# Kernel tuning notes

Measured on AMD Instinct MI355X. Metric: run time of the kernel, lower is better.

The kernel has to match this reference:

```python
import jax, jax.numpy as jnp
import numpy as np

B = 8192          # batch rows
F0 = 2048         # base input features
E = 512           # embed rows added per recursion level
L = 3             # chain depth
OUT = 2048        # MAIN output dim
NNZ_E = 8192      # nnz per embed sparse weight (~16/row)
NNZ_M = 16384     # nnz of MAIN sparse weight (~8/row)


def _spmm_t(rows, cols, vals, x, n_rows):
    """Compute (W_sparse @ x.T).T = x @ W.T for COO W of shape [n_rows, x.shape[1]].
    out[b, r] = sum_{k: rows[k]==r} vals[k] * x[b, cols[k]]
    """
    contrib = x[:, cols] * vals                     # [B, nnz]
    return jax.ops.segment_sum(contrib.T, rows, num_segments=n_rows).T  # [B, n_rows]


def setup_inputs() -> dict:
    key = jax.random.key(0)
    ks = jax.random.split(key, 12)
    widths = [F0, F0 + E, F0 + 2 * E]               # input width at each recursion level
    inp = {"x": jax.random.normal(ks[0], (B, F0), dtype=jnp.float32)}
    for i, w in enumerate(widths):
        inp[f"emb_rows{i}"] = jax.random.randint(ks[1 + 3 * i], (NNZ_E,), 0, E, dtype=jnp.int32)
        inp[f"emb_cols{i}"] = jax.random.randint(ks[2 + 3 * i], (NNZ_E,), 0, w, dtype=jnp.int32)
        inp[f"emb_vals{i}"] = jax.random.normal(ks[3 + 3 * i], (NNZ_E,), dtype=jnp.float32)
    inp["main_rows"] = jax.random.randint(ks[10], (NNZ_M,), 0, OUT, dtype=jnp.int32)
    inp["main_cols"] = jax.random.randint(ks[11], (NNZ_M,), 0, F0 + 3 * E, dtype=jnp.int32)
    inp["main_vals"] = jax.random.normal(jax.random.fold_in(key, 99), (NNZ_M,), dtype=jnp.float32)
    return inp


def reference(x, emb_rows0, emb_cols0, emb_vals0,
              emb_rows1, emb_cols1, emb_vals1,
              emb_rows2, emb_cols2, emb_vals2,
              main_rows, main_cols, main_vals):
    # Recursive chain unrolled oldest-first: each level sparse-mms its embed
    # weight against the running input and concatenates the result.
    h = x
    for rows, cols, vals in ((emb_rows0, emb_cols0, emb_vals0),
                             (emb_rows1, emb_cols1, emb_vals1),
                             (emb_rows2, emb_cols2, emb_vals2)):
        e = _spmm_t(rows, cols, vals, h, E)         # [B, E]
        h = jnp.concatenate([h, e], axis=1)
    # is_last: pass concatenated features through the MAIN sparse linear
    return _spmm_t(main_rows, main_cols, main_vals, h, OUT)  # [B, OUT]
```

## Files before the change

### kernel.cpp

```cpp
#include <hip/hip_runtime.h>
#include <stdint.h>

#define F0    2048
#define EROWS 512
#define NOUT  2048
#define MROWS 8192

typedef __attribute__((ext_vector_type(8))) short bf16x8;
typedef __attribute__((ext_vector_type(4))) float f32x4;
typedef __attribute__((ext_vector_type(8))) unsigned short u16x8;

typedef const __attribute__((address_space(1))) unsigned char ga_t;
typedef __attribute__((address_space(3))) unsigned char lds_t;

__device__ __forceinline__ void async_load16(const void* g, void* l) {
  __builtin_amdgcn_global_load_lds((ga_t*)g, (lds_t*)l, 16, 0, 0);
}

__device__ __forceinline__ unsigned short f2bf(float f) {
  unsigned int u = __builtin_bit_cast(unsigned int, f);
  u += 0x7fffu + ((u >> 16) & 1u);
  return (unsigned short)(u >> 16);
}

__global__ __launch_bounds__(256) void csr_cast_kernel(
    const int* __restrict__ r0, const int* __restrict__ c0, const float* __restrict__ v0, int n0,
    const int* __restrict__ r1, const int* __restrict__ c1, const float* __restrict__ v1, int n1,
    const int* __restrict__ r2, const int* __restrict__ c2, const float* __restrict__ v2, int n2,
    const int* __restrict__ rm, const int* __restrict__ cm, const float* __restrict__ vm, int nm,
    int* __restrict__ rp_all, int* __restrict__ cc_all, float* __restrict__ cv_all,
    const float* __restrict__ x, unsigned short* __restrict__ Ab)
{
  const int b = blockIdx.x;
  const int tid = threadIdx.x;

  if (b >= 4) {
    const int cb = b - 4;
    const float4* xp = (const float4*)x;
    u16x8* ap = (u16x8*)Ab;
#pragma unroll
    for (int it = 0; it < 4; ++it) {
      int i = cb * 1024 + it * 256 + tid;
      float4 a = xp[2 * i], c = xp[2 * i + 1];
      u16x8 o;
      o[0] = f2bf(a.x); o[1] = f2bf(a.y); o[2] = f2bf(a.z); o[3] = f2bf(a.w);
      o[4] = f2bf(c.x); o[5] = f2bf(c.y); o[6] = f2bf(c.z); o[7] = f2bf(c.w);
      ap[i] = o;
    }
    return;
  }

  const int* rows; const int* cols; const float* vals; int nnz, nrows;
  if      (b == 0) { rows = r0; cols = c0; vals = v0; nnz = n0; nrows = EROWS; }
  else if (b == 1) { rows = r1; cols = c1; vals = v1; nnz = n1; nrows = EROWS; }
  else if (b == 2) { rows = r2; cols = c2; vals = v2; nnz = n2; nrows = EROWS; }
  else             { rows = rm; cols = cm; vals = vm; nnz = nm; nrows = NOUT; }
  int* rp  = rp_all + b * 4096;
  int* cc  = cc_all + b * 8192;
  float* cv = cv_all + b * 8192;

  __shared__ int hist[NOUT + 1];
  __shared__ int tsum[256];

  for (int i = tid; i < nrows; i += 256) hist[i] = 0;
  __syncthreads();

  int k0 = 0;
  for (; k0 + 2048 <= nnz; k0 += 2048) {
    const int kk = k0 + tid * 8;
    int4 ra = *(const int4*)(rows + kk);
    int4 rb = *(const int4*)(rows + kk + 4);
    atomicAdd(&hist[ra.x], 1); atomicAdd(&hist[ra.y], 1);
    atomicAdd(&hist[ra.z], 1); atomicAdd(&hist[ra.w], 1);
    atomicAdd(&hist[rb.x], 1); atomicAdd(&hist[rb.y], 1);
    atomicAdd(&hist[rb.z], 1); atomicAdd(&hist[rb.w], 1);
  }
  for (int k = k0 + tid; k < nnz; k += 256) atomicAdd(&hist[rows[k]], 1);
  __syncthreads();

  const int per = nrows >> 8;
  const int base = tid * per;
  int sum = 0;
  for (int i = 0; i < per; ++i) sum += hist[base + i];
  tsum[tid] = sum;
  __syncthreads();
  for (int off = 1; off < 256; off <<= 1) {
    int add = (tid >= off) ? tsum[tid - off] : 0;
    __syncthreads();
    tsum[tid] += add;
    __syncthreads();
  }
  int run = (tid == 0) ? 0 : tsum[tid - 1];
  for (int i = 0; i < per; ++i) { int h = hist[base + i]; hist[base + i] = run; run += h; }
  __syncthreads();

  for (int i = tid; i < nrows; i += 256) rp[i] = hist[i];
  if (tid == 0) rp[nrows] = nnz;
  __syncthreads();

  k0 = 0;
  for (; k0 + 2048 <= nnz; k0 += 2048) {
    const int kk = k0 + tid * 8;
    int4   ra = *(const int4*)(rows + kk);
    int4   rb = *(const int4*)(rows + kk + 4);
    int4   ca = *(const int4*)(cols + kk);
    int4   cb2 = *(const int4*)(cols + kk + 4);
    float4 va = *(const float4*)(vals + kk);
    float4 vb = *(const float4*)(vals + kk + 4);
    int p;
    p = atomicAdd(&hist[ra.x], 1); cc[p] = ca.x;  cv[p] = va.x;
    p = atomicAdd(&hist[ra.y], 1); cc[p] = ca.y;  cv[p] = va.y;
    p = atomicAdd(&hist[ra.z], 1); cc[p] = ca.z;  cv[p] = va.z;
    p = atomicAdd(&hist[ra.w], 1); cc[p] = ca.w;  cv[p] = va.w;
    p = atomicAdd(&hist[rb.x], 1); cc[p] = cb2.x; cv[p] = vb.x;
    p = atomicAdd(&hist[rb.y], 1); cc[p] = cb2.y; cv[p] = vb.y;
    p = atomicAdd(&hist[rb.z], 1); cc[p] = cb2.z; cv[p] = vb.z;
    p = atomicAdd(&hist[rb.w], 1); cc[p] = cb2.w; cv[p] = vb.w;
  }
  for (int k = k0 + tid; k < nnz; k += 256) {
    int p = atomicAdd(&hist[rows[k]], 1);
    cc[p] = cols[k]; cv[p] = vals[k];
  }
}

template <bool BF16OUT>
__global__ __launch_bounds__(256) void expand_csr_kernel(
    const int* __restrict__ rp, const int* __restrict__ cc,
    const float* __restrict__ cv, const float* __restrict__ Dsrc,
    void* __restrict__ out)
{
  const int r = blockIdx.x;
  const int tid = threadIdx.x;
  __shared__ float acc[F0];
  __shared__ int   icol[128];
  __shared__ float ival[128];
  __shared__ int   icnt;

  float4* a4 = (float4*)acc;
  a4[tid * 2]     = (float4){0.f, 0.f, 0.f, 0.f};
  a4[tid * 2 + 1] = (float4){0.f, 0.f, 0.f, 0.f};
  if (tid == 0) icnt = 0;
  __syncthreads();

  const int s = rp[r], e = rp[r + 1];
  for (int i = s + tid; i < e; i += 256) {
    int c = cc[i]; float v = cv[i];
    if (c < F0) atomicAdd(&acc[c], v);
    else { int p = atomicAdd(&icnt, 1); if (p < 128) { icol[p] = c - F0; ival[p] = v; } }
  }
  __syncthreads();
  int n = icnt; if (n > 128) n = 128;

  float4 q0 = a4[tid * 2], q1 = a4[tid * 2 + 1];
  for (int j = 0; j < n; ++j) {
    const float4* src = (const float4*)(Dsrc + (size_t)icol[j] * F0) + tid * 2;
    float v = ival[j];
    float4 s0 = src[0], s1 = src[1];
    q0.x += v * s0.x; q0.y += v * s0.y; q0.z += v * s0.z; q0.w += v * s0.w;
    q1.x += v * s1.x; q1.y += v * s1.y; q1.z += v * s1.z; q1.w += v * s1.w;
  }

  if (BF16OUT) {
    u16x8 o;
    o[0] = f2bf(q0.x); o[1] = f2bf(q0.y); o[2] = f2bf(q0.z); o[3] = f2bf(q0.w);
    o[4] = f2bf(q1.x); o[5] = f2bf(q1.y); o[6] = f2bf(q1.z); o[7] = f2bf(q1.w);
    ((u16x8*)out)[(size_t)r * 256 + tid] = o;
  } else {
    float4* dst = (float4*)out + (size_t)r * 512 + tid * 2;
    dst[0] = q0; dst[1] = q1;
  }
}

__global__ __launch_bounds__(256) void gemm_bt_kernel(
    const unsigned short* __restrict__ A, const unsigned short* __restrict__ B,
    float* __restrict__ C)
{
  constexpr int K = F0;
  constexpr int N = NOUT;
  __shared__ __align__(16) unsigned short sA[128 * 64];
  __shared__ __align__(16) unsigned short sB[128 * 64];

  const int tid  = threadIdx.x;
  const int lane = tid & 63;
  const int w    = tid >> 6;
  const int wm   = (w & 1) * 64;
  const int wn   = (w >> 1) * 64;
  const int mm   = lane & 15;
  const int g    = lane >> 4;
  const int bm   = blockIdx.y;
  const int bn   = blockIdx.x;

  const unsigned short* Ag = A + (size_t)bm * 128 * K;
  const unsigned short* Bg = B + (size_t)bn * 128 * K;

  int su[4], srow[4], scg[4];
  for (int i = 0; i < 4; ++i) {
    int u = i * 256 + tid;
    su[i]   = u;
    srow[i] = u >> 3;
    scg[i]  = (u & 7) ^ ((u >> 3) & 7);
  }

  f32x4 acc[4][4];
  for (int a = 0; a < 4; ++a)
    for (int b2 = 0; b2 < 4; ++b2) acc[a][b2] = (f32x4)0.f;

  for (int k0 = 0; k0 < K; k0 += 64) {
    for (int i = 0; i < 4; ++i) {
      async_load16(Ag + (size_t)srow[i] * K + k0 + scg[i] * 8, sA + su[i] * 8);
      async_load16(Bg + (size_t)srow[i] * K + k0 + scg[i] * 8, sB + su[i] * 8);
    }
    __syncthreads();

    for (int ks = 0; ks < 2; ++ks) {
      bf16x8 af[4], bf[4];
      for (int t = 0; t < 4; ++t) {
        int mrow = wm + t * 16 + mm;
        int sa   = (ks * 4 + g) ^ (mrow & 7);
        af[t] = *(const bf16x8*)(sA + mrow * 64 + sa * 8);
        int nrow = wn + t * 16 + mm;
        int sb   = (ks * 4 + g) ^ (nrow & 7);
        bf[t] = *(const bf16x8*)(sB + nrow * 64 + sb * 8);
      }
      for (int tm = 0; tm < 4; ++tm)
        for (int tn = 0; tn < 4; ++tn)
          acc[tm][tn] = __builtin_amdgcn_mfma_f32_16x16x32_bf16(
              af[tm], bf[tn], acc[tm][tn], 0, 0, 0);
    }
    __syncthreads();
  }

  for (int tm = 0; tm < 4; ++tm) {
    int rowb = bm * 128 + wm + tm * 16 + g * 4;
    for (int tn = 0; tn < 4; ++tn) {
      int col = bn * 128 + wn + tn * 16 + mm;
      for (int r = 0; r < 4; ++r)
        C[(size_t)(rowb + r) * N + col] = acc[tm][tn][r];
    }
  }
}

extern "C" void kernel_launch(void* const* d_in, const int* in_sizes, int n_in,
                              void* d_out, int out_size, void* d_ws, size_t ws_size,
                              hipStream_t stream)
{
  const float* x   = (const float*)d_in[0];
  const int*   er0 = (const int*)d_in[1];
  const int*   ec0 = (const int*)d_in[2];
  const float* ev0 = (const float*)d_in[3];
  const int*   er1 = (const int*)d_in[4];
  const int*   ec1 = (const int*)d_in[5];
  const float* ev1 = (const float*)d_in[6];
  const int*   er2 = (const int*)d_in[7];
  const int*   ec2 = (const int*)d_in[8];
  const float* ev2 = (const float*)d_in[9];
  const int*   mr  = (const int*)d_in[10];
  const int*   mc  = (const int*)d_in[11];
  const float* mv  = (const float*)d_in[12];
  const int nnz_e0 = in_sizes[1];
  const int nnz_e1 = in_sizes[4];
  const int nnz_e2 = in_sizes[7];
  const int nnz_m  = in_sizes[10];

  int*   rp_all = (int*)d_ws;
  int*   cc_all = rp_all + 4 * 4096;
  float* cv_all = (float*)(cc_all + 48 * 1024);
  float* D      = (float*)(cv_all + 48 * 1024);
  unsigned short* Mb = (unsigned short*)(D + (size_t)3 * EROWS * F0);
  unsigned short* Ab = Mb + (size_t)NOUT * F0;

  hipLaunchKernelGGL(csr_cast_kernel, dim3(4 + 2048), dim3(256), 0, stream,
                     er0, ec0, ev0, nnz_e0,
                     er1, ec1, ev1, nnz_e1,
                     er2, ec2, ev2, nnz_e2,
                     mr,  mc,  mv,  nnz_m,
                     rp_all, cc_all, cv_all, x, Ab);

  hipLaunchKernelGGL((expand_csr_kernel<false>), dim3(EROWS), dim3(256), 0, stream,
                     rp_all + 0 * 4096, cc_all + 0 * 8192, cv_all + 0 * 8192,
                     D, (void*)D);
  hipLaunchKernelGGL((expand_csr_kernel<false>), dim3(EROWS), dim3(256), 0, stream,
                     rp_all + 1 * 4096, cc_all + 1 * 8192, cv_all + 1 * 8192,
                     D, (void*)(D + (size_t)EROWS * F0));
  hipLaunchKernelGGL((expand_csr_kernel<false>), dim3(EROWS), dim3(256), 0, stream,
                     rp_all + 2 * 4096, cc_all + 2 * 8192, cv_all + 2 * 8192,
                     D, (void*)(D + (size_t)2 * EROWS * F0));
  hipLaunchKernelGGL((expand_csr_kernel<true>), dim3(NOUT), dim3(256), 0, stream,
                     rp_all + 3 * 4096, cc_all + 3 * 8192, cv_all + 3 * 8192,
                     D, (void*)Mb);

  hipLaunchKernelGGL(gemm_bt_kernel, dim3(NOUT / 128, MROWS / 128), dim3(256),
                     0, stream, Ab, Mb, (float*)d_out);
}
```

Before: 263.6 us.

## Replace GEMM with 256x256-tile double-buffered pipelined MFMA kernel

```diff
diff --git a/kernel.cpp b/kernel.cpp
--- a/kernel.cpp
+++ b/kernel.cpp
@@ -171,73 +171,150 @@
   }
 }
 
-__global__ __launch_bounds__(256) void gemm_bt_kernel(
+__global__ __launch_bounds__(512, 2) void gemm256_kernel(
     const unsigned short* __restrict__ A, const unsigned short* __restrict__ B,
     float* __restrict__ C)
 {
-  constexpr int K = F0;
-  constexpr int N = NOUT;
-  __shared__ __align__(16) unsigned short sA[128 * 64];
-  __shared__ __align__(16) unsigned short sB[128 * 64];
+  constexpr int K  = F0;
+  constexpr int N  = NOUT;
+  constexpr int NT = K / 64;
+
+  extern __shared__ __align__(16) unsigned short lds[];
+  unsigned short* sA = lds;
+  unsigned short* sB = lds + 32768;
 
   const int tid  = threadIdx.x;
   const int lane = tid & 63;
   const int w    = tid >> 6;
-  const int wm   = (w & 1) * 64;
-  const int wn   = (w >> 1) * 64;
+  const int wr   = w >> 2;
+  const int wc   = w & 3;
   const int mm   = lane & 15;
   const int g    = lane >> 4;
+  const int sx   = mm & 7;
   const int bm   = blockIdx.y;
   const int bn   = blockIdx.x;
 
-  const unsigned short* Ag = A + (size_t)bm * 128 * K;
-  const unsigned short* Bg = B + (size_t)bn * 128 * K;
-
-  int su[4], srow[4], scg[4];
-  for (int i = 0; i < 4; ++i) {
-    int u = i * 256 + tid;
-    su[i]   = u;
-    srow[i] = u >> 3;
-    scg[i]  = (u & 7) ^ ((u >> 3) & 7);
-  }
-
-  f32x4 acc[4][4];
-  for (int a = 0; a < 4; ++a)
-    for (int b2 = 0; b2 < 4; ++b2) acc[a][b2] = (f32x4)0.f;
-
-  for (int k0 = 0; k0 < K; k0 += 64) {
-    for (int i = 0; i < 4; ++i) {
-      async_load16(Ag + (size_t)srow[i] * K + k0 + scg[i] * 8, sA + su[i] * 8);
-      async_load16(Bg + (size_t)srow[i] * K + k0 + scg[i] * 8, sB + su[i] * 8);
+  const unsigned short* Ag = A + (size_t)bm * 256 * K;
+  const unsigned short* Bg = B + (size_t)bn * 256 * K;
+
+  const int    r0    = tid >> 3;
+  const int    c0    = (tid & 7) ^ (r0 & 7);
+  const size_t goff0 = (size_t)r0 * K + c0 * 8;
+  const size_t goff1 = goff0 + (size_t)64 * K;
+  const int    loff0 = tid * 8;
+  const int    loff1 = 4096 + tid * 8;
+
+#define STG(Gb, Sb, buf, h, t) do {                                           \
+    async_load16((Gb) + goff0 + (size_t)(h) * 128 * K + (t) * 64,             \
+                 (Sb) + (buf) * 16384 + (h) * 8192 + loff0);                  \
+    async_load16((Gb) + goff1 + (size_t)(h) * 128 * K + (t) * 64,             \
+                 (Sb) + (buf) * 16384 + (h) * 8192 + loff1);                  \
+  } while (0)
+
+  const unsigned short* paB = sA + (wr * 128 + mm) * 64;
+  const unsigned short* pbB = sB + (wc * 64  + mm) * 64;
+  const int s0 = ((0 * 4 + g) ^ sx) * 8;
+  const int s1 = ((1 * 4 + g) ^ sx) * 8;
+
+  bf16x8 af[4][2];
+  bf16x8 bf0[2][2];
+  bf16x8 bf1[2][2];
+
+#define LDA(buf, qm) do {                                                     \
+    const unsigned short* p_ = paB + (buf) * 16384 + (qm) * 4096;             \
+    _Pragma("unroll") for (int tm = 0; tm < 4; ++tm) {                        \
+      af[tm][0] = *(const bf16x8*)(p_ + tm * 1024 + s0);                      \
+      af[tm][1] = *(const bf16x8*)(p_ + tm * 1024 + s1);                      \
+    } } while (0)
+
+#define LDB(dst, buf, qn) do {                                                \
+    const unsigned short* p_ = pbB + (buf) * 16384 + (qn) * 2048;             \
+    _Pragma("unroll") for (int tn = 0; tn < 2; ++tn) {                        \
+      dst[tn][0] = *(const bf16x8*)(p_ + tn * 1024 + s0);                     \
+      dst[tn][1] = *(const bf16x8*)(p_ + tn * 1024 + s1);                     \
+    } } while (0)
+
+#define PH_MFMA(qm, qn, bfX) do {                                             \
+    __builtin_amdgcn_s_setprio(1);                                            \
+    _Pragma("unroll") for (int tm = 0; tm < 4; ++tm)                          \
+    _Pragma("unroll") for (int tn = 0; tn < 2; ++tn) {                        \
+      acc[(qm)*4+tm][(qn)*2+tn] = __builtin_amdgcn_mfma_f32_16x16x32_bf16(    \
+          af[tm][0], bfX[tn][0], acc[(qm)*4+tm][(qn)*2+tn], 0, 0, 0);         \
+      acc[(qm)*4+tm][(qn)*2+tn] = __builtin_amdgcn_mfma_f32_16x16x32_bf16(    \
+          af[tm][1], bfX[tn][1], acc[(qm)*4+tm][(qn)*2+tn], 0, 0, 0);         \
+    }                                                                         \
+    __builtin_amdgcn_s_setprio(0);                                            \
+  } while (0)
+
+#define BAR        __builtin_amdgcn_s_barrier()
+#define LGKM0      asm volatile("s_waitcnt lgkmcnt(0)" ::: "memory")
+#define WAIT_VM(n) asm volatile("s_waitcnt vmcnt(" #n ")" ::: "memory")
+
+  f32x4 acc[8][4];
+#pragma unroll
+  for (int i = 0; i < 8; ++i)
+#pragma unroll
+    for (int j = 0; j < 4; ++j) acc[i][j] = (f32x4)0.f;
+
+  STG(Ag, sA, 0, 0, 0); STG(Ag, sA, 0, 1, 0);
+  STG(Bg, sB, 0, 0, 0); STG(Bg, sB, 0, 1, 0);
+  STG(Bg, sB, 1, 0, 1); STG(Bg, sB, 1, 1, 1);
+  STG(Ag, sA, 1, 0, 1);
+  WAIT_VM(6);
+  BAR;
+
+#pragma unroll 2
+  for (int t = 0; t < NT; ++t) {
+    const int buf  = t & 1;
+    const int nbuf = buf ^ 1;
+
+    LDA(buf, 0); LDB(bf0, buf, 0);
+    if (t + 1 < NT) STG(Ag, sA, nbuf, 1, t + 1);
+    BAR; LGKM0;
+    PH_MFMA(0, 0, bf0);
+    BAR;
+
+    LDB(bf1, buf, 1);
+    BAR; LGKM0;
+    PH_MFMA(0, 1, bf1);
+    BAR;
+
+    LDA(buf, 1);
+    if (t + 2 < NT) STG(Bg, sB, buf, 0, t + 2);
+    BAR; LGKM0;
+    PH_MFMA(1, 1, bf1);
+    BAR;
+
+    if (t + 2 < NT) { STG(Bg, sB, buf, 1, t + 2);
+                      STG(Ag, sA, buf, 0, t + 2); }
+    BAR;
+    PH_MFMA(1, 0, bf0);
+    if      (t + 2 < NT) { WAIT_VM(6); }
+    else if (t + 1 < NT) { WAIT_VM(0); }
+    BAR;
+  }
+
+  const int rowb = bm * 256 + wr * 128 + g * 4;
+  const int colb = bn * 256 + wc * 64 + mm;
+#pragma unroll
+  for (int im = 0; im < 8; ++im) {
+#pragma unroll
+    for (int in2 = 0; in2 < 4; ++in2) {
+      const int row = rowb + im * 16;
+      const int col = colb + in2 * 16;
+#pragma unroll
+      for (int r = 0; r < 4; ++r)
+        C[(size_t)(row + r) * N + col] = acc[im][in2][r];
     }
-    __syncthreads();
-
-    for (int ks = 0; ks < 2; ++ks) {
-      bf16x8 af[4], bf[4];
-      for (int t = 0; t < 4; ++t) {
-        int mrow = wm + t * 16 + mm;
-        int sa   = (ks * 4 + g) ^ (mrow & 7);
-        af[t] = *(const bf16x8*)(sA + mrow * 64 + sa * 8);
-        int nrow = wn + t * 16 + mm;
-        int sb   = (ks * 4 + g) ^ (nrow & 7);
-        bf[t] = *(const bf16x8*)(sB + nrow * 64 + sb * 8);
-      }
-      for (int tm = 0; tm < 4; ++tm)
-        for (int tn = 0; tn < 4; ++tn)
-          acc[tm][tn] = __builtin_amdgcn_mfma_f32_16x16x32_bf16(
-              af[tm], bf[tn], acc[tm][tn], 0, 0, 0);
-    }
-    __syncthreads();
-  }
-
-  for (int tm = 0; tm < 4; ++tm) {
-    int rowb = bm * 128 + wm + tm * 16 + g * 4;
-    for (int tn = 0; tn < 4; ++tn) {
-      int col = bn * 128 + wn + tn * 16 + mm;
-      for (int r = 0; r < 4; ++r)
-        C[(size_t)(rowb + r) * N + col] = acc[tm][tn][r];
-    }
-  }
+  }
+
+#undef STG
+#undef LDA
+#undef LDB
+#undef PH_MFMA
+#undef BAR
+#undef LGKM0
+#undef WAIT_VM
 }
 
 extern "C" void kernel_launch(void* const* d_in, const int* in_sizes, int n_in,
@@ -289,6 +366,8 @@
                      rp_all + 3 * 4096, cc_all + 3 * 8192, cv_all + 3 * 8192,
                      D, (void*)Mb);
 
-  hipLaunchKernelGGL(gemm_bt_kernel, dim3(NOUT / 128, MROWS / 128), dim3(256),
-                     0, stream, Ab, Mb, (float*)d_out);
-}
+  hipFuncSetAttribute(reinterpret_cast<const void*>(gemm256_kernel),
+                      hipFuncAttributeMaxDynamicSharedMemorySize, 131072);
+  hipLaunchKernelGGL(gemm256_kernel, dim3(NOUT / 256, MROWS / 256), dim3(512),
+                     131072, stream, Ab, Mb, (float*)d_out);
+}
```

Result: faster. 240.3 us (-8.9%).
